# Performance work log

Measured on AMD Instinct MI355X. Metric: run time of the kernel, lower is better.

The kernel has to match this reference:

```python
import jax, jax.numpy as jnp
import numpy as np

NEG_SLOPE = 0.01  # PyTorch LeakyReLU default


def leaky(x):
    return jnp.where(x >= 0, x, NEG_SLOPE * x)


def conv(x, w, b, stride, pad):
    # x: NCHW, w: OIHW
    y = jax.lax.conv_general_dilated(
        x, w, (stride, stride), [(pad, pad), (pad, pad)],
        dimension_numbers=("NCHW", "OIHW", "NCHW"))
    return y + b[None, :, None, None]


def conv_transpose(x, w, b, stride, pad):
    # w has PyTorch ConvTranspose2d layout (in, out, kh, kw)
    wf = jnp.flip(w, (2, 3)).transpose(1, 0, 2, 3)  # -> (out, in, kh, kw)
    k = w.shape[2]
    p = k - 1 - pad
    y = jax.lax.conv_general_dilated(
        x, wf, (1, 1), [(p, p), (p, p)], lhs_dilation=(stride, stride),
        dimension_numbers=("NCHW", "OIHW", "NCHW"))
    return y + b[None, :, None, None]


def setup_inputs() -> dict:
    key = jax.random.key(0)
    ks = jax.random.split(key, 16)
    D, K = 64, 512
    s = 0.05
    inp = {
        "x": jax.random.normal(ks[0], (64, 1, 128, 128), jnp.float32),
        # encoder
        "ew1": jax.random.normal(ks[1], (8, 1, 4, 4), jnp.float32) * s,
        "eb1": jnp.zeros((8,), jnp.float32),
        "ew2": jax.random.normal(ks[2], (16, 8, 4, 4), jnp.float32) * s,
        "eb2": jnp.zeros((16,), jnp.float32),
        "ew3": jax.random.normal(ks[3], (16, 16, 3, 3), jnp.float32) * s,
        "eb3": jnp.zeros((16,), jnp.float32),
        "ew4": jax.random.normal(ks[4], (D, 16, 1, 1), jnp.float32) * s,
        "eb4": jnp.zeros((D,), jnp.float32),
        # codebook, init uniform(-1/K, 1/K) as in the module
        "codebook": jax.random.uniform(ks[5], (K, D), jnp.float32, -1.0 / K, 1.0 / K),
        # decoder
        "dw1": jax.random.normal(ks[6], (16, D, 3, 3), jnp.float32) * s,
        "db1": jnp.zeros((16,), jnp.float32),
        "dw2": jax.random.normal(ks[7], (16, 8, 4, 4), jnp.float32) * s,  # ConvT (in,out,k,k)
        "db2": jnp.zeros((8,), jnp.float32),
        "dw3": jax.random.normal(ks[8], (8, 1, 4, 4), jnp.float32) * s,  # ConvT (in,out,k,k)
        "db3": jnp.zeros((1,), jnp.float32),
    }
    return inp


BETA = 0.25


def vq(latents_nchw, codebook):
    # latents -> NHWC
    lat = jnp.transpose(latents_nchw, (0, 2, 3, 1))
    shp = lat.shape
    D = shp[-1]
    flat = lat.reshape(-1, D)  # [M, D]
    # pairwise squared distances to codebook [M, K]
    dist = (jnp.sum(flat ** 2, axis=1, keepdims=True)
            + jnp.sum(codebook ** 2, axis=1)
            - 2.0 * flat @ codebook.T)
    inds = jnp.argmin(dist, axis=1)  # [M]
    quant = codebook[inds].reshape(shp)  # gather == one-hot @ codebook
    commitment_loss = jnp.mean((jax.lax.stop_gradient(quant) - lat) ** 2)
    embedding_loss = jnp.mean((quant - jax.lax.stop_gradient(lat)) ** 2)
    vq_loss = commitment_loss * BETA + embedding_loss
    # straight-through estimator
    quant = lat + jax.lax.stop_gradient(quant - lat)
    return jnp.transpose(quant, (0, 3, 1, 2)), vq_loss


def reference(x, ew1, eb1, ew2, eb2, ew3, eb3, ew4, eb4, codebook,
              dw1, db1, dw2, db2, dw3, db3):
    # encoder
    h = leaky(conv(x, ew1, eb1, 2, 1))
    h = leaky(conv(h, ew2, eb2, 2, 1))
    h = leaky(conv(h, ew3, eb3, 1, 1))
    h = leaky(conv(h, ew4, eb4, 1, 0))
    # vector quantization
    q, vq_loss = vq(h, codebook)
    # decoder
    d = leaky(conv(q, dw1, db1, 1, 1))
    d = leaky(conv_transpose(d, dw2, db2, 2, 1))
    d = jnp.tanh(conv_transpose(d, dw3, db3, 2, 1))
    return d, vq_loss
```

## Files before the change

kernel.cpp:

```cpp
#include <hip/hip_runtime.h>
#include <math.h>

#define DEV __device__ __forceinline__
DEV float leakyf(float v) { return v >= 0.f ? v : 0.01f * v; }
DEV int rfl(int v) { return __builtin_amdgcn_readfirstlane(v); }

#define OFF_A    0u
#define OFF_B    2097152u
#define OFF_C    3145728u
#define OFF_D1   8388608u
#define OFF_D2   9437184u
#define OFF_IDX  11534336u
#define OFF_U    11599872u
#define OFF_C2   11673600u
#define OFF_W4T  11674112u
#define OFF_DWT  11675136u
#define OFF_LOSS 11684352u

__global__ void prep_k(const float* __restrict__ ew4, const float* __restrict__ dw1,
                       const float* __restrict__ cb, float* __restrict__ ws)
{
    int b = blockIdx.x, t = threadIdx.x;
    if (b < 4) {
        int id = b * 256 + t;
        int d = id & 63, ci = id >> 6;
        ws[OFF_W4T + id] = ew4[d * 16 + ci];
    } else if (b < 6) {
        int k = (b - 4) * 256 + t;
        float s = 0.f;
        #pragma unroll
        for (int d = 0; d < 64; ++d) { float v = cb[k * 64 + d]; s = fmaf(v, v, s); }
        ws[OFF_C2 + k] = s;
    } else {
        int id = (b - 6) * 256 + t;
        if (id < 9216) {
            int co = id & 15, tap = (id >> 4) % 9, ci = id / 144;
            ws[OFF_DWT + id] = dw1[(co * 64 + ci) * 9 + tap];
        }
    }
}

__global__ void uprep_k(const float* __restrict__ dwT, const float* __restrict__ cb,
                        float* __restrict__ U)
{
    int id = blockIdx.x * 256 + threadIdx.x;
    int k = id / 144;
    int r = id - k * 144;
    float s = 0.f;
    #pragma unroll
    for (int ci = 0; ci < 64; ++ci)
        s = fmaf(cb[k * 64 + ci], dwT[ci * 144 + r], s);
    U[id] = s;
}

template<int CIN, int COUT, int COB, int K, int S, int P, int HIN, int HOUT>
__global__ __launch_bounds__(256) void convf_k(const float* __restrict__ in,
                                               const float* __restrict__ w,
                                               const float* __restrict__ b,
                                               float* __restrict__ out)
{
    constexpr int NCG = COUT / COB;
    constexpr int WSZ = CIN * K * K * COB;
    __shared__ float wl[WSZ];
    int t = threadIdx.x;
    int idx = blockIdx.x * 256 + t;
    int x  = idx % HOUT;
    int y  = (idx / HOUT) % HOUT;
    int cg = (idx / (HOUT * HOUT)) % NCG;
    int n  = idx / (HOUT * HOUT * NCG);

    for (int i = t; i < WSZ; i += 256) {
        int co = i % COB;
        int r  = i / COB;
        int kx = r % K, ky = (r / K) % K, ci = r / (K * K);
        wl[i] = w[(((cg * COB + co) * CIN + ci) * K + ky) * K + kx];
    }
    __syncthreads();

    float acc[COB];
    #pragma unroll
    for (int j = 0; j < COB; ++j) acc[j] = b[cg * COB + j];

    const float* inn = in + n * CIN * HIN * HIN;
    for (int ci = 0; ci < CIN; ++ci) {
        #pragma unroll
        for (int ky = 0; ky < K; ++ky) {
            int iy = y * S - P + ky;
            bool vy = (iy >= 0) && (iy < HIN);
            #pragma unroll
            for (int kx = 0; kx < K; ++kx) {
                int ix = x * S - P + kx;
                float v = (vy && ix >= 0 && ix < HIN) ? inn[(ci * HIN + iy) * HIN + ix] : 0.f;
                const float* wp = &wl[((ci * K + ky) * K + kx) * COB];
                if constexpr (COB % 4 == 0) {
                    #pragma unroll
                    for (int j4 = 0; j4 < COB / 4; ++j4) {
                        float4 wv = *(const float4*)(wp + j4 * 4);
                        acc[j4 * 4 + 0] = fmaf(v, wv.x, acc[j4 * 4 + 0]);
                        acc[j4 * 4 + 1] = fmaf(v, wv.y, acc[j4 * 4 + 1]);
                        acc[j4 * 4 + 2] = fmaf(v, wv.z, acc[j4 * 4 + 2]);
                        acc[j4 * 4 + 3] = fmaf(v, wv.w, acc[j4 * 4 + 3]);
                    }
                } else {
                    #pragma unroll
                    for (int j = 0; j < COB; ++j) acc[j] = fmaf(v, wp[j], acc[j]);
                }
            }
        }
    }
    #pragma unroll
    for (int j = 0; j < COB; ++j)
        out[((n * COUT + cg * COB + j) * HOUT + y) * HOUT + x] = leakyf(acc[j]);
}

template<int CIN, int COUT, int COB, int K, int S, int P, int HIN, int HOUT, int ACT>
__global__ __launch_bounds__(256) void convtf_k(const float* __restrict__ in,
                                                const float* __restrict__ w,
                                                const float* __restrict__ b,
                                                float* __restrict__ out)
{
    constexpr int NCG = COUT / COB;
    constexpr int WSZ = CIN * K * K * COB;
    constexpr int NTAP = K / S;
    __shared__ float wl[WSZ];
    int t = threadIdx.x;
    int idx = blockIdx.x * 256 + t;
    int x  = idx % HOUT;
    int y  = (idx / HOUT) % HOUT;
    int cg = (idx / (HOUT * HOUT)) % NCG;
    int n  = idx / (HOUT * HOUT * NCG);

    for (int i = t; i < WSZ; i += 256) {
        int co = i % COB;
        int r  = i / COB;
        int kx = r % K, ky = (r / K) % K, ci = r / (K * K);
        wl[i] = w[((ci * COUT + cg * COB + co) * K + ky) * K + kx];
    }
    __syncthreads();

    float acc[COB];
    #pragma unroll
    for (int j = 0; j < COB; ++j) acc[j] = b[cg * COB + j];

    int py = (y + P) % S;
    int px = (x + P) % S;
    const float* inn = in + n * CIN * HIN * HIN;
    for (int ci = 0; ci < CIN; ++ci) {
        #pragma unroll
        for (int ty = 0; ty < NTAP; ++ty) {
            int ky = py + ty * S;
            int iy = (y + P - ky) / S;
            bool vy = (ky < K) && (iy >= 0) && (iy < HIN);
            #pragma unroll
            for (int tx = 0; tx < NTAP; ++tx) {
                int kx = px + tx * S;
                int ix = (x + P - kx) / S;
                float v = (vy && kx < K && ix >= 0 && ix < HIN)
                              ? inn[(ci * HIN + iy) * HIN + ix] : 0.f;
                const float* wp = &wl[((ci * K + ky) * K + kx) * COB];
                if constexpr (COB % 4 == 0) {
                    #pragma unroll
                    for (int j4 = 0; j4 < COB / 4; ++j4) {
                        float4 wv = *(const float4*)(wp + j4 * 4);
                        acc[j4 * 4 + 0] = fmaf(v, wv.x, acc[j4 * 4 + 0]);
                        acc[j4 * 4 + 1] = fmaf(v, wv.y, acc[j4 * 4 + 1]);
                        acc[j4 * 4 + 2] = fmaf(v, wv.z, acc[j4 * 4 + 2]);
                        acc[j4 * 4 + 3] = fmaf(v, wv.w, acc[j4 * 4 + 3]);
                    }
                } else {
                    #pragma unroll
                    for (int j = 0; j < COB; ++j) acc[j] = fmaf(v, wp[j], acc[j]);
                }
            }
        }
    }
    #pragma unroll
    for (int j = 0; j < COB; ++j) {
        float r = acc[j];
        out[((n * COUT + cg * COB + j) * HOUT + y) * HOUT + x] =
            (ACT == 0) ? leakyf(r) : tanhf(r);
    }
}

__global__ __launch_bounds__(256) void vqh_k(const float* __restrict__ h3,
                                             const float* __restrict__ w4t,
                                             const float* __restrict__ eb4,
                                             const float* __restrict__ cb,
                                             const float* __restrict__ c2,
                                             int* __restrict__ idxOut,
                                             float* __restrict__ lossAcc)
{
    __shared__ float Fs[8192];
    __shared__ float Cs[8192];
    int t = threadIdx.x;
    int row0 = blockIdx.x << 7;
    int n = row0 >> 10;
    int pos0 = row0 & 1023;

    {
        int row = t & 127, dh = t >> 7;
        const float* hp = h3 + (n << 14) + pos0 + row;
        float h[16];
        #pragma unroll
        for (int ci = 0; ci < 16; ++ci) h[ci] = hp[ci << 10];
        int rot = ((row >> 3) & 7) << 2;
        #pragma unroll
        for (int q = 0; q < 8; ++q) {
            int d0 = dh * 32 + q * 4;
            float a0 = eb4[d0 + 0], a1 = eb4[d0 + 1];
            float a2 = eb4[d0 + 2], a3 = eb4[d0 + 3];
            #pragma unroll
            for (int ci = 0; ci < 16; ++ci) {
                float v = h[ci];
                const float* wp = w4t + (ci << 6) + d0;
                a0 = fmaf(v, wp[0], a0); a1 = fmaf(v, wp[1], a1);
                a2 = fmaf(v, wp[2], a2); a3 = fmaf(v, wp[3], a3);
            }
            float4 wv = { leakyf(a0), leakyf(a1), leakyf(a2), leakyf(a3) };
            *(float4*)&Fs[(row << 6) + (d0 ^ rot)] = wv;
        }
    }

    int tr = t & 15, tc = t >> 4;
    int rotF = (tr & 7) << 2;
    int rotC = (tc & 7) << 2;
    float best[8]; int bk[8];
    #pragma unroll
    for (int i = 0; i < 8; ++i) { best[i] = 3.4e38f; bk[i] = 0; }

    #pragma unroll 1
    for (int p = 0; p < 4; ++p) {
        __syncthreads();
        {
            int code = t >> 1, dh = t & 1;
            int kk = (p << 7) + code;
            int rot = ((code >> 3) & 7) << 2;
            const float* src = cb + (kk << 6);
            #pragma unroll
            for (int q = 0; q < 8; ++q) {
                int d0 = dh * 32 + q * 4;
                *(float4*)&Cs[(code << 6) + (d0 ^ rot)] = *(const float4*)(src + d0);
            }
        }
        __syncthreads();

        float acc[8][8];
        #pragma unroll
        for (int i = 0; i < 8; ++i)
            #pragma unroll
            for (int j = 0; j < 8; ++j) acc[i][j] = 0.f;

        #pragma unroll 1
        for (int dc = 0; dc < 16; ++dc) {
            int d0 = dc << 2;
            float4 fv[8];
            #pragma unroll
            for (int i = 0; i < 8; ++i)
                fv[i] = *(const float4*)&Fs[((tr * 8 + i) << 6) + (d0 ^ rotF)];
            #pragma unroll
            for (int j = 0; j < 8; ++j) {
                float4 cv = *(const float4*)&Cs[((tc * 8 + j) << 6) + (d0 ^ rotC)];
                #pragma unroll
                for (int i = 0; i < 8; ++i) {
                    acc[i][j] = fmaf(fv[i].x, cv.x, acc[i][j]);
                    acc[i][j] = fmaf(fv[i].y, cv.y, acc[i][j]);
                    acc[i][j] = fmaf(fv[i].z, cv.z, acc[i][j]);
                    acc[i][j] = fmaf(fv[i].w, cv.w, acc[i][j]);
                }
            }
        }
        #pragma unroll
        for (int j = 0; j < 8; ++j) {
            int kk = (p << 7) + tc * 8 + j;
            float hc2 = 0.5f * c2[kk];
            #pragma unroll
            for (int i = 0; i < 8; ++i) {
                float s = hc2 - acc[i][j];
                if (s < best[i]) { best[i] = s; bk[i] = kk; }
            }
        }
    }

    __syncthreads();
    float* redS = Cs;
    int*   redI = (int*)(Cs + 2176);
    #pragma unroll
    for (int i = 0; i < 8; ++i) {
        int row = tr * 8 + i;
        redS[row * 17 + tc] = best[i];
        redI[row * 17 + tc] = bk[i];
    }
    __syncthreads();
    if (t < 128) {
        int row = t;
        float bs = redS[row * 17]; int bi = redI[row * 17];
        #pragma unroll
        for (int c = 1; c < 16; ++c) {
            float s2 = redS[row * 17 + c];
            int   i2 = redI[row * 17 + c];
            if (s2 < bs || (s2 == bs && i2 < bi)) { bs = s2; bi = i2; }
        }
        idxOut[row0 + row] = bi;
        int rot = ((row >> 3) & 7) << 2;
        const float* cr = cb + (bi << 6);
        float rs = 0.f;
        #pragma unroll
        for (int q = 0; q < 16; ++q) {
            int d0 = q * 4;
            float4 fv = *(const float4*)&Fs[(row << 6) + (d0 ^ rot)];
            float e0 = cr[d0 + 0] - fv.x, e1 = cr[d0 + 1] - fv.y;
            float e2 = cr[d0 + 2] - fv.z, e3 = cr[d0 + 3] - fv.w;
            rs = fmaf(e0, e0, rs); rs = fmaf(e1, e1, rs);
            rs = fmaf(e2, e2, rs); rs = fmaf(e3, e3, rs);
        }
        #pragma unroll
        for (int off = 32; off; off >>= 1) rs += __shfl_down(rs, off, 64);
        if ((t & 63) == 0) atomicAdd(lossAcc, rs);
    }
}

__global__ __launch_bounds__(256) void d1_k(const int* __restrict__ idx,
                                            const float* __restrict__ U,
                                            const float* __restrict__ db1,
                                            float* __restrict__ out)
{
    int id = blockIdx.x * 256 + threadIdx.x;
    int x = id & 31, y = (id >> 5) & 31;
    int cg = rfl((id >> 10) & 3), n = id >> 12;
    float acc[4];
    #pragma unroll
    for (int j = 0; j < 4; ++j) acc[j] = db1[cg * 4 + j];
    const float4* U4 = (const float4*)U;
    #pragma unroll
    for (int tap = 0; tap < 9; ++tap) {
        int yy = y + tap / 3 - 1, xx = x + tap % 3 - 1;
        if (yy < 0 || yy > 31 || xx < 0 || xx > 31) continue;
        int k = idx[(n << 10) + (yy << 5) + xx];
        float4 u = U4[(k * 9 + tap) * 4 + cg];
        acc[0] += u.x; acc[1] += u.y; acc[2] += u.z; acc[3] += u.w;
    }
    #pragma unroll
    for (int j = 0; j < 4; ++j)
        out[((n * 16 + cg * 4 + j) << 10) + (y << 5) + x] = leakyf(acc[j]);
}

__global__ void loss_k(const float* __restrict__ acc, float* __restrict__ out)
{
    out[0] = 1.25f * acc[0] / 4194304.0f;
}

extern "C" void kernel_launch(void* const* d_in, const int* in_sizes, int n_in,
                              void* d_out, int out_size, void* d_ws, size_t ws_size,
                              hipStream_t stream)
{
    const float* x        = (const float*)d_in[0];
    const float* ew1      = (const float*)d_in[1];
    const float* eb1      = (const float*)d_in[2];
    const float* ew2      = (const float*)d_in[3];
    const float* eb2      = (const float*)d_in[4];
    const float* ew3      = (const float*)d_in[5];
    const float* eb3      = (const float*)d_in[6];
    const float* ew4      = (const float*)d_in[7];
    const float* eb4      = (const float*)d_in[8];
    const float* codebook = (const float*)d_in[9];
    const float* dw1      = (const float*)d_in[10];
    const float* db1      = (const float*)d_in[11];
    const float* dw2      = (const float*)d_in[12];
    const float* db2      = (const float*)d_in[13];
    const float* dw3      = (const float*)d_in[14];
    const float* db3      = (const float*)d_in[15];

    float* out = (float*)d_out;
    float* ws  = (float*)d_ws;
    float* A    = ws + OFF_A;
    float* B    = ws + OFF_B;
    float* C    = ws + OFF_C;
    float* D1   = ws + OFF_D1;
    float* D2   = ws + OFF_D2;
    int*   IDX  = (int*)(ws + OFF_IDX);
    float* U    = ws + OFF_U;
    float* C2   = ws + OFF_C2;
    float* W4T  = ws + OFF_W4T;
    float* DWT  = ws + OFF_DWT;
    float* LOSS = ws + OFF_LOSS;

    hipMemsetAsync(LOSS, 0, sizeof(float), stream);
    prep_k<<<42, 256, 0, stream>>>(ew4, dw1, codebook, ws);
    uprep_k<<<288, 256, 0, stream>>>(DWT, codebook, U);

    convf_k<1, 8, 8, 4, 2, 1, 128, 64><<<1024, 256, 0, stream>>>(x, ew1, eb1, A);
    convf_k<8, 16, 4, 4, 2, 1, 64, 32><<<1024, 256, 0, stream>>>(A, ew2, eb2, B);
    convf_k<16, 16, 4, 3, 1, 1, 32, 32><<<1024, 256, 0, stream>>>(B, ew3, eb3, C);

    vqh_k<<<512, 256, 0, stream>>>(C, W4T, eb4, codebook, C2, IDX, LOSS);

    d1_k<<<1024, 256, 0, stream>>>(IDX, U, db1, D1);
    convtf_k<16, 8, 8, 4, 2, 1, 32, 64, 0><<<1024, 256, 0, stream>>>(D1, dw2, db2, D2);
    convtf_k<8, 1, 1, 4, 2, 1, 64, 128, 1><<<4096, 256, 0, stream>>>(D2, dw3, db3, out);

    loss_k<<<1, 1, 0, stream>>>(LOSS, out + 1048576);
}
```

Before: 162.0 us.

## Transpose VQ shared-memory tiles to dimension-major layout for outer-product GEMM

Stores the latent and codebook tiles in LDS as [dim][row] instead of row-major with XOR swizzling. The distance GEMM becomes a per-dimension outer product that reads two float4s from each tile per step, and each thread's rows and codes are split into two groups of four. The goal is fewer LDS loads per FMA and simpler addressing. In exchange, the LDS stores during tile fill become scalar and strided, which may cause bank conflicts, and the final loss loop reads LDS with scalar accesses.

```diff
diff --git a/kernel.cpp b/kernel.cpp
--- a/kernel.cpp
+++ b/kernel.cpp
@@ -190,8 +190,8 @@
                                              int* __restrict__ idxOut,
                                              float* __restrict__ lossAcc)
 {
-    __shared__ float Fs[8192];
-    __shared__ float Cs[8192];
+    __shared__ float Fs[64 * 128];
+    __shared__ float Cs[64 * 128];
     int t = threadIdx.x;
     int row0 = blockIdx.x << 7;
     int n = row0 >> 10;
@@ -203,7 +203,6 @@
         float h[16];
         #pragma unroll
         for (int ci = 0; ci < 16; ++ci) h[ci] = hp[ci << 10];
-        int rot = ((row >> 3) & 7) << 2;
         #pragma unroll
         for (int q = 0; q < 8; ++q) {
             int d0 = dh * 32 + q * 4;
@@ -216,14 +215,14 @@
                 a0 = fmaf(v, wp[0], a0); a1 = fmaf(v, wp[1], a1);
                 a2 = fmaf(v, wp[2], a2); a3 = fmaf(v, wp[3], a3);
             }
-            float4 wv = { leakyf(a0), leakyf(a1), leakyf(a2), leakyf(a3) };
-            *(float4*)&Fs[(row << 6) + (d0 ^ rot)] = wv;
+            Fs[(d0 + 0) * 128 + row] = leakyf(a0);
+            Fs[(d0 + 1) * 128 + row] = leakyf(a1);
+            Fs[(d0 + 2) * 128 + row] = leakyf(a2);
+            Fs[(d0 + 3) * 128 + row] = leakyf(a3);
         }
     }
 
     int tr = t & 15, tc = t >> 4;
-    int rotF = (tr & 7) << 2;
-    int rotC = (tc & 7) << 2;
     float best[8]; int bk[8];
     #pragma unroll
     for (int i = 0; i < 8; ++i) { best[i] = 3.4e38f; bk[i] = 0; }
@@ -233,13 +232,15 @@
         __syncthreads();
         {
             int code = t >> 1, dh = t & 1;
-            int kk = (p << 7) + code;
-            int rot = ((code >> 3) & 7) << 2;
-            const float* src = cb + (kk << 6);
+            const float* src = cb + (((p << 7) + code) << 6) + dh * 32;
             #pragma unroll
             for (int q = 0; q < 8; ++q) {
+                float4 v = *(const float4*)(src + q * 4);
                 int d0 = dh * 32 + q * 4;
-                *(float4*)&Cs[(code << 6) + (d0 ^ rot)] = *(const float4*)(src + d0);
+                Cs[(d0 + 0) * 128 + code] = v.x;
+                Cs[(d0 + 1) * 128 + code] = v.y;
+                Cs[(d0 + 2) * 128 + code] = v.z;
+                Cs[(d0 + 3) * 128 + code] = v.w;
             }
         }
         __syncthreads();
@@ -250,28 +251,27 @@
             #pragma unroll
             for (int j = 0; j < 8; ++j) acc[i][j] = 0.f;
 
-        #pragma unroll 1
-        for (int dc = 0; dc < 16; ++dc) {
-            int d0 = dc << 2;
-            float4 fv[8];
+        const float* fp0 = &Fs[tr * 4];
+        const float* fp1 = &Fs[64 + tr * 4];
+        const float* cp0 = &Cs[tc * 4];
+        const float* cp1 = &Cs[64 + tc * 4];
+        #pragma unroll 8
+        for (int d = 0; d < 64; ++d) {
+            float4 f0 = *(const float4*)(fp0 + d * 128);
+            float4 f1 = *(const float4*)(fp1 + d * 128);
+            float4 c0 = *(const float4*)(cp0 + d * 128);
+            float4 c1 = *(const float4*)(cp1 + d * 128);
+            float f[8] = { f0.x, f0.y, f0.z, f0.w, f1.x, f1.y, f1.z, f1.w };
+            float c[8] = { c0.x, c0.y, c0.z, c0.w, c1.x, c1.y, c1.z, c1.w };
             #pragma unroll
             for (int i = 0; i < 8; ++i)
-                fv[i] = *(const float4*)&Fs[((tr * 8 + i) << 6) + (d0 ^ rotF)];
-            #pragma unroll
-            for (int j = 0; j < 8; ++j) {
-                float4 cv = *(const float4*)&Cs[((tc * 8 + j) << 6) + (d0 ^ rotC)];
                 #pragma unroll
-                for (int i = 0; i < 8; ++i) {
-                    acc[i][j] = fmaf(fv[i].x, cv.x, acc[i][j]);
-                    acc[i][j] = fmaf(fv[i].y, cv.y, acc[i][j]);
-                    acc[i][j] = fmaf(fv[i].z, cv.z, acc[i][j]);
-                    acc[i][j] = fmaf(fv[i].w, cv.w, acc[i][j]);
-                }
-            }
+                for (int j = 0; j < 8; ++j)
+                    acc[i][j] = fmaf(f[i], c[j], acc[i][j]);
         }
         #pragma unroll
         for (int j = 0; j < 8; ++j) {
-            int kk = (p << 7) + tc * 8 + j;
+            int kk = (p << 7) + (j < 4 ? tc * 4 + j : 64 + tc * 4 + j - 4);
             float hc2 = 0.5f * c2[kk];
             #pragma unroll
             for (int i = 0; i < 8; ++i) {
@@ -286,7 +286,7 @@
     int*   redI = (int*)(Cs + 2176);
     #pragma unroll
     for (int i = 0; i < 8; ++i) {
-        int row = tr * 8 + i;
+        int row = (i < 4) ? tr * 4 + i : 64 + tr * 4 + i - 4;
         redS[row * 17 + tc] = best[i];
         redI[row * 17 + tc] = bk[i];
     }
@@ -301,17 +301,12 @@
             if (s2 < bs || (s2 == bs && i2 < bi)) { bs = s2; bi = i2; }
         }
         idxOut[row0 + row] = bi;
-        int rot = ((row >> 3) & 7) << 2;
         const float* cr = cb + (bi << 6);
         float rs = 0.f;
         #pragma unroll
-        for (int q = 0; q < 16; ++q) {
-            int d0 = q * 4;
-            float4 fv = *(const float4*)&Fs[(row << 6) + (d0 ^ rot)];
-            float e0 = cr[d0 + 0] - fv.x, e1 = cr[d0 + 1] - fv.y;
-            float e2 = cr[d0 + 2] - fv.z, e3 = cr[d0 + 3] - fv.w;
-            rs = fmaf(e0, e0, rs); rs = fmaf(e1, e1, rs);
-            rs = fmaf(e2, e2, rs); rs = fmaf(e3, e3, rs);
+        for (int d = 0; d < 64; ++d) {
+            float e = cr[d] - Fs[d * 128 + row];
+            rs = fmaf(e, e, rs);
         }
         #pragma unroll
         for (int off = 32; off; off >>= 1) rs += __shfl_down(rs, off, 64);
```

New measurement: 148.9 us. 1.09x faster.
